# Performance work log

Hardware: AMD Instinct MI355X
Metric: run time of the kernel (lower is better)

## Reference

```python
import jax, jax.numpy as jnp
import numpy as np

N_OBS, N_DIM, N_FUNCTIONS, N_APPLICATIONS = 65536, 256, 16, 8


def setup_inputs() -> dict:
    key = jax.random.key(0)
    k1, k2, k3, k4 = jax.random.split(key, 4)
    x = jax.random.normal(k1, (N_OBS, N_DIM), dtype=jnp.float32)
    function_indices = jax.random.randint(k2, (N_OBS, N_APPLICATIONS), 0, N_FUNCTIONS, dtype=jnp.int32)
    # Stacked Dense weights/biases, one per IFS function. Scale keeps column
    # norms well under the MaxNorm(0.99) constraint (contractive maps).
    W = jax.random.normal(k3, (N_FUNCTIONS, N_DIM, N_DIM), dtype=jnp.float32) * 0.05
    b = jax.random.normal(k4, (N_FUNCTIONS, N_DIM), dtype=jnp.float32) * 0.05
    return {"x": x, "function_indices": function_indices, "W": W, "b": b}


def reference(x, function_indices, W, b):
    # One IFS application step: compute all n_functions affine maps for every
    # point (as the original layer does), then select the per-point function.
    def step(carry, idx):
        # carry: (n_obs, n_dim); idx: (n_obs,) int
        y_all = jnp.einsum('od,fde->ofe', carry, W) + b  # (n_obs, n_funcs, n_dim)
        y = jnp.take_along_axis(y_all, idx[:, None, None].astype(jnp.int32), axis=1)[:, 0, :]
        return y, None
    # scan over the n_applications axis (leading axis after transpose)
    out, _ = jax.lax.scan(step, x, function_indices.T)
    return out
```

## Files before the change

kernel.cpp:

```cpp
#include <hip/hip_runtime.h>
#include <hip/hip_bf16.h>
#include <stdint.h>

#define N_OBS 65536
#define N_DIM 256
#define N_FUN 16
#define N_APP 8
#define MT 64
#define STRIDE 66560
#define MAXT 1040
#define N_BLK 256

typedef __attribute__((ext_vector_type(8))) short v8s;
typedef __attribute__((ext_vector_type(4))) short v4s;
typedef __attribute__((ext_vector_type(4))) float v4f;

__device__ __forceinline__ unsigned short f2bf(float f) {
  union { float f; uint32_t u; } v;
  v.f = f;
  uint32_t u = v.u;
  return (unsigned short)((u + 0x7FFFu + ((u >> 16) & 1u)) >> 16);
}

__device__ __forceinline__ int xcd_swz(int bid, int n) {
  int q = n >> 3;
  return (bid & 7) * q + (bid >> 3);
}

__global__ void k_init(int* __restrict__ perm, int total) {
  int tid = blockIdx.x * 256 + threadIdx.x;
  if (tid < total) perm[tid] = -1;
}

__global__ void k_prep_w(const float* __restrict__ W, unsigned short* __restrict__ Wt) {
  int tid = blockIdx.x * 256 + threadIdx.x;
  int f = tid >> 16, n = (tid >> 8) & 255, k = tid & 255;
  Wt[tid] = f2bf(W[(f << 16) | (k << 8) | n]);
}

__global__ void k_hist(const int* __restrict__ fidx, int* __restrict__ blockCnt) {
  __shared__ int h[N_APP * N_FUN];
  int tid = threadIdx.x;
  if (tid < N_APP * N_FUN) h[tid] = 0;
  __syncthreads();
  size_t o = blockIdx.x * 256 + tid;
  const int4* p = (const int4*)(fidx + o * 8);
  int4 a = p[0], b = p[1];
  atomicAdd(&h[0 * N_FUN + a.x], 1);
  atomicAdd(&h[1 * N_FUN + a.y], 1);
  atomicAdd(&h[2 * N_FUN + a.z], 1);
  atomicAdd(&h[3 * N_FUN + a.w], 1);
  atomicAdd(&h[4 * N_FUN + b.x], 1);
  atomicAdd(&h[5 * N_FUN + b.y], 1);
  atomicAdd(&h[6 * N_FUN + b.z], 1);
  atomicAdd(&h[7 * N_FUN + b.w], 1);
  __syncthreads();
  if (tid < N_APP * N_FUN) blockCnt[tid * N_BLK + blockIdx.x] = h[tid];
}

__global__ void k_tot(const int* __restrict__ blockCnt, int* __restrict__ tot) {
  __shared__ int s[256];
  int tid = threadIdx.x;
  s[tid] = blockCnt[blockIdx.x * N_BLK + tid];
  __syncthreads();
  for (int o = 128; o > 0; o >>= 1) {
    if (tid < o) s[tid] += s[tid + o];
    __syncthreads();
  }
  if (tid == 0) tot[blockIdx.x] = s[0];
}

__global__ void k_base(const int* __restrict__ tot, int* __restrict__ pb,
                       int* __restrict__ tilef) {
  __shared__ int pbl[N_APP * 17];
  int tid = threadIdx.x;
  if (tid < N_APP) {
    int base = 0;
    for (int f = 0; f < N_FUN; ++f) {
      pbl[tid * 17 + f] = base;
      int c = tot[tid * N_FUN + f];
      base += (c + MT - 1) & ~(MT - 1);
    }
    pbl[tid * 17 + 16] = base;
  }
  __syncthreads();
  if (tid < N_APP * 17) pb[tid] = pbl[tid];
  for (int idx = tid; idx < N_APP * MAXT; idx += 256) {
    int t = idx / MAXT, q = idx - t * MAXT;
    int posn = q * MT;
    int fg = 0;
    #pragma unroll
    for (int f = 1; f < N_FUN; ++f)
      if (posn >= pbl[t * 17 + f]) fg = f;
    tilef[idx] = fg;
  }
}

__global__ void k_off(const int* __restrict__ blockCnt, const int* __restrict__ pb,
                      int* __restrict__ blockOff) {
  __shared__ int s[256];
  int bin = blockIdx.x, tid = threadIdx.x;
  int c = blockCnt[bin * N_BLK + tid];
  s[tid] = c;
  __syncthreads();
  for (int o = 1; o < 256; o <<= 1) {
    int v = (tid >= o) ? s[tid - o] : 0;
    __syncthreads();
    s[tid] += v;
    __syncthreads();
  }
  int t = bin >> 4, f = bin & 15;
  blockOff[bin * N_BLK + tid] = pb[t * 17 + f] + s[tid] - c;
}

__global__ void k_scatter(const int* __restrict__ fidx, const int* __restrict__ blockOff,
                          int* __restrict__ perm) {
  __shared__ int cur[N_APP * N_FUN];
  int tid = threadIdx.x;
  if (tid < N_APP * N_FUN) cur[tid] = blockOff[tid * N_BLK + blockIdx.x];
  __syncthreads();
  size_t o = blockIdx.x * 256 + tid;
  const int4* p = (const int4*)(fidx + o * 8);
  int4 a = p[0], b = p[1];
  int fs[8] = {a.x, a.y, a.z, a.w, b.x, b.y, b.z, b.w};
  #pragma unroll
  for (int t = 0; t < N_APP; ++t) {
    int pos = atomicAdd(&cur[t * N_FUN + fs[t]], 1);
    perm[t * STRIDE + pos] = (int)o;
  }
}

__global__ void k_pos(const int* __restrict__ perm, int* __restrict__ pos) {
  int tid = blockIdx.x * 256 + threadIdx.x;
  if (tid >= 7 * STRIDE) return;
  int t = tid / STRIDE + 1, s = tid - (t - 1) * STRIDE;
  int o = perm[t * STRIDE + s];
  if (o >= 0) pos[(t - 1) * N_OBS + o] = s;
}

__global__ void k_outpos(int* __restrict__ perm, const int* __restrict__ pos,
                         int* __restrict__ outpos0) {
  int tid = blockIdx.x * 256 + threadIdx.x;
  if (tid >= 7 * STRIDE) return;
  int t = tid / STRIDE, s = tid - t * STRIDE;
  int o = perm[t * STRIDE + s];
  int val = (o >= 0) ? pos[t * N_OBS + o] : -1;
  if (t == 0) outpos0[s] = val;
  else perm[t * STRIDE + s] = val;
}

template <int SRC_F32, int DST_F32>
__global__ __launch_bounds__(256, 2)
void k_step(const void* __restrict__ src_, void* __restrict__ dst_,
            const unsigned short* __restrict__ Wt, const float* __restrict__ bias,
            const int* __restrict__ pb_t, const int* __restrict__ tilef_t,
            const int* __restrict__ outpos_t, const int* __restrict__ perm0) {
  int tid = threadIdx.x;
  int tile = xcd_swz(blockIdx.x, gridDim.x);
  if (tile * MT >= pb_t[16]) return;
  int f = tilef_t[tile];
  int lane = tid & 63, wave = tid >> 6, l15 = lane & 15, lq = lane >> 4;
  int cb = wave << 6;
  int rowbase = tile * MT;

  const unsigned short* Wf =
      Wt + ((size_t)f << 16) + ((size_t)(cb + l15) << 8) + (lq << 3);
  v8s b[4][8];
  #pragma unroll
  for (int nt = 0; nt < 4; ++nt)
    #pragma unroll
    for (int kk = 0; kk < 8; ++kk)
      b[nt][kk] = *(const v8s*)(Wf + (nt << 12) + (kk << 5));
  #pragma unroll
  for (int nt = 0; nt < 4; ++nt)
    #pragma unroll
    for (int kk = 0; kk < 8; ++kk)
      asm volatile("" : "+v"(b[nt][kk]));

  #pragma unroll
  for (int g = 0; g < 4; ++g) {
    int mrow = rowbase + (g << 4) + l15;
    v8s a[8];
    if (SRC_F32) {
      int grow = perm0[mrow];
      if (grow < 0) grow = 0;
      const float* xr = (const float*)src_ + ((size_t)grow << 8) + (lq << 3);
      #pragma unroll
      for (int kk = 0; kk < 8; ++kk) {
        v4f v0 = *(const v4f*)(xr + kk * 32);
        v4f v1 = *(const v4f*)(xr + kk * 32 + 4);
        v8s t;
        t[0] = (short)f2bf(v0[0]); t[1] = (short)f2bf(v0[1]);
        t[2] = (short)f2bf(v0[2]); t[3] = (short)f2bf(v0[3]);
        t[4] = (short)f2bf(v1[0]); t[5] = (short)f2bf(v1[1]);
        t[6] = (short)f2bf(v1[2]); t[7] = (short)f2bf(v1[3]);
        a[kk] = t;
      }
    } else {
      const unsigned short* sr =
          (const unsigned short*)src_ + ((size_t)mrow << 8) + (lq << 3);
      #pragma unroll
      for (int kk = 0; kk < 8; ++kk)
        a[kk] = *(const v8s*)(sr + kk * 32);
    }

    v4f acc[4] = {};
    #pragma unroll
    for (int kk = 0; kk < 8; ++kk) {
      #pragma unroll
      for (int nt = 0; nt < 4; ++nt)
        acc[nt] = __builtin_amdgcn_mfma_f32_16x16x32_bf16(b[nt][kk], a[kk], acc[nt], 0, 0, 0);
    }

    int op = outpos_t[mrow];
    if (op >= 0) {
      const float* bf_ = bias + (f << 8) + cb + (lq << 2);
      if (DST_F32) {
        float* dr = (float*)dst_ + ((size_t)op << 8) + cb + (lq << 2);
        #pragma unroll
        for (int nt = 0; nt < 4; ++nt) {
          v4f bv = *(const v4f*)(bf_ + (nt << 4));
          v4f o = acc[nt] + bv;
          *(v4f*)(dr + (nt << 4)) = o;
        }
      } else {
        unsigned short* dr = (unsigned short*)dst_ + ((size_t)op << 8) + cb + (lq << 2);
        #pragma unroll
        for (int nt = 0; nt < 4; ++nt) {
          v4f bv = *(const v4f*)(bf_ + (nt << 4));
          v4s pk;
          pk[0] = (short)f2bf(acc[nt][0] + bv[0]);
          pk[1] = (short)f2bf(acc[nt][1] + bv[1]);
          pk[2] = (short)f2bf(acc[nt][2] + bv[2]);
          pk[3] = (short)f2bf(acc[nt][3] + bv[3]);
          *(v4s*)(dr + (nt << 4)) = pk;
        }
      }
    }
  }
}

extern "C" void kernel_launch(void* const* d_in, const int* in_sizes, int n_in,
                              void* d_out, int out_size, void* d_ws, size_t ws_size,
                              hipStream_t stream) {
  const float* x = (const float*)d_in[0];
  const int* fidx = (const int*)d_in[1];
  const float* W = (const float*)d_in[2];
  const float* bias = (const float*)d_in[3];
  char* ws = (char*)d_ws;

  unsigned short* carryA = (unsigned short*)ws;
  int* blockCnt = (int*)ws;
  int* blockOff = (int*)(ws + 131072);
  int* tot      = (int*)(ws + 262144);
  int* pos      = (int*)(ws + 262656);
  unsigned short* Wt = (unsigned short*)(ws + 34078720);
  int* perm    = (int*)(ws + 36175872);
  int* pb      = (int*)(ws + 38305792);
  int* tilef   = (int*)(ws + 38306336);
  int* outpos0 = (int*)(ws + 38339616);
  unsigned short* carryB = (unsigned short*)d_out;

  k_init<<<(N_APP * STRIDE + 255) / 256, 256, 0, stream>>>(perm, N_APP * STRIDE);
  k_prep_w<<<(N_FUN * 65536) / 256, 256, 0, stream>>>(W, Wt);
  k_hist<<<N_BLK, 256, 0, stream>>>(fidx, blockCnt);
  k_tot<<<128, 256, 0, stream>>>(blockCnt, tot);
  k_base<<<1, 256, 0, stream>>>(tot, pb, tilef);
  k_off<<<128, 256, 0, stream>>>(blockCnt, pb, blockOff);
  k_scatter<<<N_BLK, 256, 0, stream>>>(fidx, blockOff, perm);
  k_pos<<<(7 * STRIDE + 255) / 256, 256, 0, stream>>>(perm, pos);
  k_outpos<<<(7 * STRIDE + 255) / 256, 256, 0, stream>>>(perm, pos, outpos0);

  k_step<1, 0><<<MAXT, 256, 0, stream>>>(x, carryA, Wt, bias, pb, tilef, outpos0, perm);
  for (int t = 1; t < 7; ++t) {
    const unsigned short* s = (t & 1) ? carryA : carryB;
    unsigned short* d = (t & 1) ? carryB : carryA;
    k_step<0, 0><<<MAXT, 256, 0, stream>>>(
        s, d, Wt, bias, pb + t * 17, tilef + t * MAXT, perm + t * STRIDE, nullptr);
  }
  k_step<0, 1><<<MAXT, 256, 0, stream>>>(
      carryA, d_out, Wt, bias, pb + 7 * 17, tilef + 7 * MAXT, perm + 7 * STRIDE, nullptr);
}
```

Before: 459.7 us.

## Stage activation tile in swizzled LDS and stream weights per k-step

Each block now loads its 64-row activation tile into shared memory, using direct global-to-LDS loads for bf16 intermediates and converted loads for the f32 input. It uses an XOR-swizzled layout in LDS, and the intermediate carry buffer in global memory is written in the same swizzled per-tile layout. Weight fragments are no longer held in registers for the whole kernel; they are read from global memory per k-step, and each one is reused across four row sub-tiles. Occupancy is raised from two to five blocks per CU. This cuts register pressure and redundant activation reads, at the cost of 32KB of LDS per block, a barrier, and repeated weight loads that rely on cache.

Result: slower. 665.9 us (+44.8%).

```diff
diff --git a/kernel.cpp b/kernel.cpp
--- a/kernel.cpp
+++ b/kernel.cpp
@@ -150,91 +150,95 @@
 }
 
 template <int SRC_F32, int DST_F32>
-__global__ __launch_bounds__(256, 2)
+__global__ __launch_bounds__(256, 5)
 void k_step(const void* __restrict__ src_, void* __restrict__ dst_,
             const unsigned short* __restrict__ Wt, const float* __restrict__ bias,
             const int* __restrict__ pb_t, const int* __restrict__ tilef_t,
             const int* __restrict__ outpos_t, const int* __restrict__ perm0) {
+  __shared__ unsigned short As[MT * N_DIM];
   int tid = threadIdx.x;
   int tile = xcd_swz(blockIdx.x, gridDim.x);
   if (tile * MT >= pb_t[16]) return;
   int f = tilef_t[tile];
   int lane = tid & 63, wave = tid >> 6, l15 = lane & 15, lq = lane >> 4;
-  int cb = wave << 6;
-  int rowbase = tile * MT;
-
-  const unsigned short* Wf =
-      Wt + ((size_t)f << 16) + ((size_t)(cb + l15) << 8) + (lq << 3);
-  v8s b[4][8];
+
+  if (SRC_F32) {
+    const int* permBase = perm0 + tile * MT;
+    #pragma unroll
+    for (int i = 0; i < 8; ++i) {
+      int g0 = tid + i * 256;
+      int row = g0 >> 5, c = g0 & 31;
+      int grow = permBase[row];
+      if (grow < 0) grow = 0;
+      const v4f* s = (const v4f*)((const float*)src_ + ((size_t)grow << 8) + (c << 3));
+      v4f v0 = s[0], v1 = s[1];
+      v8s val;
+      val[0] = (short)f2bf(v0[0]); val[1] = (short)f2bf(v0[1]);
+      val[2] = (short)f2bf(v0[2]); val[3] = (short)f2bf(v0[3]);
+      val[4] = (short)f2bf(v1[0]); val[5] = (short)f2bf(v1[1]);
+      val[6] = (short)f2bf(v1[2]); val[7] = (short)f2bf(v1[3]);
+      *(v8s*)((char*)As + (row << 9) + ((c ^ (row & 7)) << 4)) = val;
+    }
+  } else {
+    const char* srcT = (const char*)src_ + ((size_t)tile << 15);
+    #pragma unroll
+    for (int i = 0; i < 8; ++i) {
+      int off = (((wave << 3) + i) << 10);
+      __builtin_amdgcn_global_load_lds(
+          (const unsigned int*)(srcT + off + (lane << 4)),
+          (unsigned int*)((char*)As + off), 16, 0, 0);
+    }
+  }
+  __syncthreads();
+
+  v4f acc[4][4] = {};
+  const unsigned short* Wf = Wt + ((size_t)f << 16);
+
   #pragma unroll
-  for (int nt = 0; nt < 4; ++nt)
-    #pragma unroll
-    for (int kk = 0; kk < 8; ++kk)
-      b[nt][kk] = *(const v8s*)(Wf + (nt << 12) + (kk << 5));
+  for (int kk = 0; kk < 8; ++kk) {
+    v8s a[4];
+    #pragma unroll
+    for (int mt = 0; mt < 4; ++mt) {
+      int row = mt * 16 + l15;
+      a[mt] = *(const v8s*)((const char*)As + (row << 9) + ((((kk << 2) + lq) ^ (row & 7)) << 4));
+    }
+    #pragma unroll
+    for (int nt = 0; nt < 4; ++nt) {
+      int n = (wave << 6) + nt * 16 + l15;
+      v8s bfr = *(const v8s*)(Wf + n * N_DIM + (kk << 5) + (lq << 3));
+      #pragma unroll
+      for (int mt = 0; mt < 4; ++mt)
+        acc[mt][nt] = __builtin_amdgcn_mfma_f32_16x16x32_bf16(bfr, a[mt], acc[mt][nt], 0, 0, 0);
+    }
+  }
+
+  const float* bf_ = bias + (f << 8) + (wave << 6) + (lq << 2);
   #pragma unroll
-  for (int nt = 0; nt < 4; ++nt)
-    #pragma unroll
-    for (int kk = 0; kk < 8; ++kk)
-      asm volatile("" : "+v"(b[nt][kk]));
-
-  #pragma unroll
-  for (int g = 0; g < 4; ++g) {
-    int mrow = rowbase + (g << 4) + l15;
-    v8s a[8];
-    if (SRC_F32) {
-      int grow = perm0[mrow];
-      if (grow < 0) grow = 0;
-      const float* xr = (const float*)src_ + ((size_t)grow << 8) + (lq << 3);
+  for (int mt = 0; mt < 4; ++mt) {
+    int op = outpos_t[tile * MT + mt * 16 + l15];
+    if (op < 0) continue;
+    if (DST_F32) {
+      float* dr = (float*)dst_ + ((size_t)op << 8) + (wave << 6) + (lq << 2);
       #pragma unroll
-      for (int kk = 0; kk < 8; ++kk) {
-        v4f v0 = *(const v4f*)(xr + kk * 32);
-        v4f v1 = *(const v4f*)(xr + kk * 32 + 4);
-        v8s t;
-        t[0] = (short)f2bf(v0[0]); t[1] = (short)f2bf(v0[1]);
-        t[2] = (short)f2bf(v0[2]); t[3] = (short)f2bf(v0[3]);
-        t[4] = (short)f2bf(v1[0]); t[5] = (short)f2bf(v1[1]);
-        t[6] = (short)f2bf(v1[2]); t[7] = (short)f2bf(v1[3]);
-        a[kk] = t;
+      for (int nt = 0; nt < 4; ++nt) {
+        v4f bv = *(const v4f*)(bf_ + (nt << 4));
+        v4f o = acc[mt][nt] + bv;
+        *(v4f*)(dr + (nt << 4)) = o;
       }
     } else {
-      const unsigned short* sr =
-          (const unsigned short*)src_ + ((size_t)mrow << 8) + (lq << 3);
+      int row = op & 63;
+      char* dt_ = (char*)dst_ + (((size_t)op >> 6) << 15) + (row << 9);
       #pragma unroll
-      for (int kk = 0; kk < 8; ++kk)
-        a[kk] = *(const v8s*)(sr + kk * 32);
-    }
-
-    v4f acc[4] = {};
-    #pragma unroll
-    for (int kk = 0; kk < 8; ++kk) {
-      #pragma unroll
-      for (int nt = 0; nt < 4; ++nt)
-        acc[nt] = __builtin_amdgcn_mfma_f32_16x16x32_bf16(b[nt][kk], a[kk], acc[nt], 0, 0, 0);
-    }
-
-    int op = outpos_t[mrow];
-    if (op >= 0) {
-      const float* bf_ = bias + (f << 8) + cb + (lq << 2);
-      if (DST_F32) {
-        float* dr = (float*)dst_ + ((size_t)op << 8) + cb + (lq << 2);
-        #pragma unroll
-        for (int nt = 0; nt < 4; ++nt) {
-          v4f bv = *(const v4f*)(bf_ + (nt << 4));
-          v4f o = acc[nt] + bv;
-          *(v4f*)(dr + (nt << 4)) = o;
-        }
-      } else {
-        unsigned short* dr = (unsigned short*)dst_ + ((size_t)op << 8) + cb + (lq << 2);
-        #pragma unroll
-        for (int nt = 0; nt < 4; ++nt) {
-          v4f bv = *(const v4f*)(bf_ + (nt << 4));
-          v4s pk;
-          pk[0] = (short)f2bf(acc[nt][0] + bv[0]);
-          pk[1] = (short)f2bf(acc[nt][1] + bv[1]);
-          pk[2] = (short)f2bf(acc[nt][2] + bv[2]);
-          pk[3] = (short)f2bf(acc[nt][3] + bv[3]);
-          *(v4s*)(dr + (nt << 4)) = pk;
-        }
+      for (int nt = 0; nt < 4; ++nt) {
+        int n0 = (wave << 6) + (nt << 4) + (lq << 2);
+        int c = n0 >> 3;
+        v4f bv = *(const v4f*)(bf_ + (nt << 4));
+        v4s pk;
+        pk[0] = (short)f2bf(acc[mt][nt][0] + bv[0]);
+        pk[1] = (short)f2bf(acc[mt][nt][1] + bv[1]);
+        pk[2] = (short)f2bf(acc[mt][nt][2] + bv[2]);
+        pk[3] = (short)f2bf(acc[mt][nt][3] + bv[3]);
+        *(v4s*)(dt_ + ((c ^ (row & 7)) << 4) + ((n0 & 7) << 1)) = pk;
       }
     }
   }
```
